# Kernel tuning notes

Measured on AMD Instinct MI355X. Metric: run time of the kernel, lower is better.

## Reference

```python
import jax, jax.numpy as jnp
import numpy as np

N_HEADS = 16
NEG_INF = -1e9


def setup_inputs() -> dict:
    key = jax.random.key(0)
    k1, k2, k3 = jax.random.split(key, 3)
    B, S, D = 4, 4096, 1024
    x = jax.random.normal(k1, (B, S, D), dtype=jnp.float32)
    # GPT-2-style init scale
    w_qkv = jax.random.normal(k2, (D, 3 * D), dtype=jnp.float32) * 0.02
    b_qkv = jnp.zeros((3 * D,), dtype=jnp.float32)
    w_o = jax.random.normal(k3, (D, D), dtype=jnp.float32) * 0.02
    b_o = jnp.zeros((D,), dtype=jnp.float32)
    return {"x": x, "w_qkv": w_qkv, "b_qkv": b_qkv, "w_o": w_o, "b_o": b_o,
            "window_size": 512}


def reference(x, w_qkv, b_qkv, w_o, b_o, window_size):
    B, S, D = x.shape
    W = window_size
    n_win = S // W  # loop `for i in range(0, S, W)` with S % W == 0
    H = N_HEADS
    dh = D // H

    # All windows are independent -> fold them into the batch dim instead of a
    # Python loop (same math as looping + concat along seq dim).
    xw = x.reshape(B * n_win, W, D)

    qkv = xw @ w_qkv + b_qkv                      # [BN, W, 3D]
    q, k, v = jnp.split(qkv, 3, axis=-1)
    # [BN, H, W, dh]
    q = q.reshape(-1, W, H, dh).transpose(0, 2, 1, 3)
    k = k.reshape(-1, W, H, dh).transpose(0, 2, 1, 3)
    v = v.reshape(-1, W, H, dh).transpose(0, 2, 1, 3)

    scale = 1.0 / jnp.sqrt(jnp.asarray(dh, dtype=x.dtype))
    scores = jnp.einsum('bhqd,bhkd->bhqk', q, k) * scale  # [BN, H, W, W]
    causal = jnp.tril(jnp.ones((W, W), dtype=bool))       # GPT-2 causal mask (per window)
    scores = jnp.where(causal, scores, NEG_INF)
    attn = jax.nn.softmax(scores, axis=-1)

    out = jnp.einsum('bhqk,bhkd->bhqd', attn, v)          # [BN, H, W, dh]
    out = out.transpose(0, 2, 1, 3).reshape(-1, W, D)     # [BN, W, D]
    out = out @ w_o + b_o
    return out.reshape(B, S, D)
```

## Files before the change

kernel.cpp:

```cpp
#include <hip/hip_runtime.h>


typedef unsigned short u16;
typedef unsigned int u32;
typedef __attribute__((ext_vector_type(8))) short bf16x8;
typedef __attribute__((ext_vector_type(4))) float f32x4;

__device__ __forceinline__ float bf2f(u16 v) {
  union { u32 u; float f; } t; t.u = ((u32)v) << 16; return t.f;
}
__device__ __forceinline__ u16 f2bf(float f) {
  union { float f; u32 u; } t; t.f = f;
  u32 u = t.u + 0x7fffu + ((t.u >> 16) & 1u);
  return (u16)(u >> 16);
}
__device__ __forceinline__ void g2lds16(const void* g, void* l) {
  __builtin_amdgcn_global_load_lds((const __attribute__((address_space(1))) void*)g,
                                   (__attribute__((address_space(3))) void*)l,
                                   16, 0, 0);
}

__global__ __launch_bounds__(256) void canon_x(
    const float* __restrict__ xf, u16* __restrict__ xb) {
  size_t i = ((size_t)blockIdx.x * 256 + threadIdx.x) * 8;
  float4 a = *(const float4*)(xf + i);
  float4 b = *(const float4*)(xf + i + 4);
  u16 o[8] = { f2bf(a.x), f2bf(a.y), f2bf(a.z), f2bf(a.w),
               f2bf(b.x), f2bf(b.y), f2bf(b.z), f2bf(b.w) };
  *(bf16x8*)(xb + i) = *(bf16x8*)o;
}

__global__ __launch_bounds__(256) void transpose_w(
    const float* __restrict__ in, u16* __restrict__ out, int R, int C) {
  __shared__ u16 tile[32][33];
  int c0 = blockIdx.x * 32, r0 = blockIdx.y * 32;
  int tx = threadIdx.x & 31, ty = threadIdx.x >> 5;
#pragma unroll
  for (int i = 0; i < 32; i += 8)
    tile[ty + i][tx] = f2bf(in[(size_t)(r0 + ty + i) * C + c0 + tx]);
  __syncthreads();
#pragma unroll
  for (int i = 0; i < 32; i += 8)
    out[(size_t)(c0 + ty + i) * R + r0 + tx] = tile[tx][ty + i];
}

__global__ __launch_bounds__(256) void transpose_v(
    const u16* __restrict__ qkv, u16* __restrict__ vt) {
  __shared__ u16 tile[32][33];
  int bh = blockIdx.z, bn = bh >> 4, h = bh & 15;
  int t0 = blockIdx.x * 32, d0 = blockIdx.y * 32;
  int tx = threadIdx.x & 31, ty = threadIdx.x >> 5;
  const u16* src = qkv + (size_t)(bn * 512) * 3072 + 2048 + h * 64;
#pragma unroll
  for (int i = 0; i < 32; i += 8)
    tile[ty + i][tx] = src[(size_t)(t0 + ty + i) * 3072 + d0 + tx];
  __syncthreads();
  u16* dst = vt + ((size_t)bh * 64 + d0) * 512 + t0;
#pragma unroll
  for (int i = 0; i < 32; i += 8)
    dst[(size_t)(ty + i) * 512 + tx] = tile[tx][ty + i];
}

template <typename OutT>
__global__ __launch_bounds__(256, 2) void gemm_bt_bias(
    const u16* __restrict__ A, const u16* __restrict__ Bt,
    const float* __restrict__ bias, OutT* __restrict__ C,
    int M, int N, int K) {
  __shared__ __align__(16) u16 As[128 * 32];
  __shared__ __align__(16) u16 Bs[128 * 32];
  const int tid = threadIdx.x;
  const int wave = tid >> 6, lane = tid & 63;
  const int quad = lane >> 4, l16 = lane & 15;
  const int m0 = blockIdx.y * 128, n0 = blockIdx.x * 128;
  const int wm = (wave >> 1) * 64, wn = (wave & 1) * 64;

  f32x4 acc[4][4] = {};

  int e0 = (wave * 512) + lane * 8;
  int e1 = 2048 + e0;
  int rA0 = e0 >> 5, cA0 = e0 & 31;
  int rA1 = e1 >> 5, cA1 = e1 & 31;
  const u16* ga0 = A + (size_t)(m0 + rA0) * K + cA0;
  const u16* ga1 = A + (size_t)(m0 + rA1) * K + cA1;
  const u16* gb0 = Bt + (size_t)(n0 + rA0) * K + cA0;
  const u16* gb1 = Bt + (size_t)(n0 + rA1) * K + cA1;
  u16* As0 = As + (size_t)wave * 512;
  u16* As1 = As0 + 2048;
  u16* Bs0 = Bs + (size_t)wave * 512;
  u16* Bs1 = Bs0 + 2048;

  for (int k0 = 0; k0 < K; k0 += 32) {
    g2lds16(ga0 + k0, As0);
    g2lds16(ga1 + k0, As1);
    g2lds16(gb0 + k0, Bs0);
    g2lds16(gb1 + k0, Bs1);
    __syncthreads();
    bf16x8 a[4], b[4];
#pragma unroll
    for (int mi = 0; mi < 4; ++mi)
      a[mi] = *(const bf16x8*)(As + (wm + mi * 16 + l16) * 32 + quad * 8);
#pragma unroll
    for (int ni = 0; ni < 4; ++ni)
      b[ni] = *(const bf16x8*)(Bs + (wn + ni * 16 + l16) * 32 + quad * 8);
#pragma unroll
    for (int mi = 0; mi < 4; ++mi)
#pragma unroll
      for (int ni = 0; ni < 4; ++ni)
        acc[mi][ni] = __builtin_amdgcn_mfma_f32_16x16x32_bf16(a[mi], b[ni], acc[mi][ni], 0, 0, 0);
    __syncthreads();
  }

#pragma unroll
  for (int ni = 0; ni < 4; ++ni) {
    int col = n0 + wn + ni * 16 + l16;
    float bv = bias[col];
#pragma unroll
    for (int mi = 0; mi < 4; ++mi) {
      int row = m0 + wm + mi * 16 + quad * 4;
#pragma unroll
      for (int r = 0; r < 4; ++r) {
        float v = acc[mi][ni][r] + bv;
        if constexpr (sizeof(OutT) == 2)
          C[(size_t)(row + r) * N + col] = f2bf(v);
        else
          C[(size_t)(row + r) * N + col] = v;
      }
    }
  }
}

__global__ __launch_bounds__(256, 2) void attn_win(
    const u16* __restrict__ qkv, const u16* __restrict__ vt,
    u16* __restrict__ attn) {
  __shared__ __align__(16) u16 Qs[128 * 64];
  __shared__ __align__(16) u16 Ks[128 * 64];
  __shared__ __align__(16) u16 Vs[64 * 128];
  __shared__ __align__(16) u16 Ps[4][32 * 128];

  const int qt = blockIdx.x, h = blockIdx.y, bn = blockIdx.z;
  const int bh = bn * 16 + h;
  const int tid = threadIdx.x;
  const int wave = tid >> 6, lane = tid & 63;
  const int quad = lane >> 4, l16 = lane & 15;
  const int t0 = bn * 512 + qt * 128;

#pragma unroll
  for (int it = 0; it < 4; ++it) {
    int i = it * 256 + tid;
    int row = i >> 3, c = i & 7;
    bf16x8 v = *(const bf16x8*)(qkv + (size_t)(t0 + row) * 3072 + h * 64 + c * 8);
    *(bf16x8*)(Qs + row * 64 + ((c ^ (row & 7)) * 8)) = v;
  }

  float mrun[2][4], lrun[2][4];
  f32x4 o[2][4] = {};
#pragma unroll
  for (int mi = 0; mi < 2; ++mi)
#pragma unroll
    for (int r = 0; r < 4; ++r) { mrun[mi][r] = -1e30f; lrun[mi][r] = 0.f; }

  const float cexp = 0.18033688011112042f;

  for (int j = 0; j <= qt; ++j) {
    int tk = bn * 512 + j * 128;
#pragma unroll
    for (int it = 0; it < 4; ++it) {
      int i = it * 256 + tid;
      int rk = i >> 3, ck = i & 7;
      bf16x8 kv = *(const bf16x8*)(qkv + (size_t)(tk + rk) * 3072 + 1024 + h * 64 + ck * 8);
      *(bf16x8*)(Ks + rk * 64 + ((ck ^ (rk & 7)) * 8)) = kv;
      int rv = i >> 4, cv = i & 15;
      bf16x8 vv = *(const bf16x8*)(vt + ((size_t)bh * 64 + rv) * 512 + j * 128 + cv * 8);
      *(bf16x8*)(Vs + rv * 128 + ((cv ^ (rv & 15)) * 8)) = vv;
    }
    __syncthreads();

    f32x4 s[2][8] = {};
#pragma unroll
    for (int ks = 0; ks < 2; ++ks) {
      bf16x8 aq[2];
#pragma unroll
      for (int mi = 0; mi < 2; ++mi) {
        int m = wave * 32 + mi * 16 + l16;
        aq[mi] = *(const bf16x8*)(Qs + m * 64 + (((ks * 4 + quad) ^ (m & 7)) * 8));
      }
#pragma unroll
      for (int ni = 0; ni < 8; ++ni) {
        int n = ni * 16 + l16;
        bf16x8 bk = *(const bf16x8*)(Ks + n * 64 + (((ks * 4 + quad) ^ (n & 7)) * 8));
        s[0][ni] = __builtin_amdgcn_mfma_f32_16x16x32_bf16(aq[0], bk, s[0][ni], 0, 0, 0);
        s[1][ni] = __builtin_amdgcn_mfma_f32_16x16x32_bf16(aq[1], bk, s[1][ni], 0, 0, 0);
      }
    }

    const bool diag = (j == qt);
#pragma unroll
    for (int mi = 0; mi < 2; ++mi) {
#pragma unroll
      for (int r = 0; r < 4; ++r) {
        int m = wave * 32 + mi * 16 + quad * 4 + r;
        float rmax = -1e30f;
#pragma unroll
        for (int ni = 0; ni < 8; ++ni) {
          float v = s[mi][ni][r] * cexp;
          if (diag && (ni * 16 + l16 > m)) v = -1e30f;
          s[mi][ni][r] = v;
          rmax = fmaxf(rmax, v);
        }
        rmax = fmaxf(rmax, __shfl_xor(rmax, 1));
        rmax = fmaxf(rmax, __shfl_xor(rmax, 2));
        rmax = fmaxf(rmax, __shfl_xor(rmax, 4));
        rmax = fmaxf(rmax, __shfl_xor(rmax, 8));
        float mnew = fmaxf(mrun[mi][r], rmax);
        float alpha = exp2f(mrun[mi][r] - mnew);
        mrun[mi][r] = mnew;
        float rsum = 0.f;
#pragma unroll
        for (int ni = 0; ni < 8; ++ni) {
          float pv = exp2f(s[mi][ni][r] - mnew);
          s[mi][ni][r] = pv;
          rsum += pv;
        }
        rsum += __shfl_xor(rsum, 1);
        rsum += __shfl_xor(rsum, 2);
        rsum += __shfl_xor(rsum, 4);
        rsum += __shfl_xor(rsum, 8);
        lrun[mi][r] = lrun[mi][r] * alpha + rsum;
#pragma unroll
        for (int di = 0; di < 4; ++di) o[mi][di][r] *= alpha;
      }
    }

    u16* pw = &Ps[wave][0];
#pragma unroll
    for (int mi = 0; mi < 2; ++mi)
#pragma unroll
      for (int ni = 0; ni < 8; ++ni)
#pragma unroll
        for (int r = 0; r < 4; ++r) {
          int row = mi * 16 + quad * 4 + r;
          int col = ni * 16 + l16;
          int phys = (col >> 3) ^ (row & 15);
          pw[row * 128 + phys * 8 + (col & 7)] = f2bf(s[mi][ni][r]);
        }
    __syncthreads();

#pragma unroll
    for (int ks = 0; ks < 4; ++ks) {
      bf16x8 ap[2];
#pragma unroll
      for (int mi = 0; mi < 2; ++mi) {
        int row = mi * 16 + l16;
        ap[mi] = *(const bf16x8*)(pw + row * 128 + (((ks * 4 + quad) ^ (row & 15)) * 8));
      }
#pragma unroll
      for (int di = 0; di < 4; ++di) {
        int n = di * 16 + l16;
        bf16x8 bv = *(const bf16x8*)(Vs + n * 128 + (((ks * 4 + quad) ^ (n & 15)) * 8));
        o[0][di] = __builtin_amdgcn_mfma_f32_16x16x32_bf16(ap[0], bv, o[0][di], 0, 0, 0);
        o[1][di] = __builtin_amdgcn_mfma_f32_16x16x32_bf16(ap[1], bv, o[1][di], 0, 0, 0);
      }
    }
    __syncthreads();
  }

#pragma unroll
  for (int mi = 0; mi < 2; ++mi)
#pragma unroll
    for (int r = 0; r < 4; ++r) {
      float inv = 1.0f / lrun[mi][r];
      int trow = t0 + wave * 32 + mi * 16 + quad * 4 + r;
#pragma unroll
      for (int di = 0; di < 4; ++di)
        attn[(size_t)trow * 1024 + h * 64 + di * 16 + l16] = f2bf(o[mi][di][r] * inv);
    }
}

extern "C" void kernel_launch(void* const* d_in, const int* in_sizes, int n_in,
                              void* d_out, int out_size, void* d_ws, size_t ws_size,
                              hipStream_t stream) {
  (void)in_sizes; (void)n_in; (void)out_size; (void)ws_size;
  const float* x     = (const float*)d_in[0];
  const float* w_qkv = (const float*)d_in[1];
  const float* b_qkv = (const float*)d_in[2];
  const float* w_o   = (const float*)d_in[3];
  const float* b_o   = (const float*)d_in[4];
  float* out = (float*)d_out;

  char* ws = (char*)d_ws;
  u16* qkv   = (u16*)(ws + 0);
  u16* vtb   = (u16*)(ws + 100663296);
  u16* attnb = (u16*)(ws + 134217728);
  u16* xb    = (u16*)(ws + 167772160);
  u16* wqkvT = (u16*)(ws + 201326592);
  u16* woT   = (u16*)(ws + 207618048);

  canon_x<<<8192, 256, 0, stream>>>(x, xb);
  transpose_w<<<dim3(96, 32), 256, 0, stream>>>(w_qkv, wqkvT, 1024, 3072);
  transpose_w<<<dim3(32, 32), 256, 0, stream>>>(w_o, woT, 1024, 1024);

  gemm_bt_bias<u16><<<dim3(24, 128), 256, 0, stream>>>(
      xb, wqkvT, b_qkv, qkv, 16384, 3072, 1024);
  transpose_v<<<dim3(16, 2, 512), 256, 0, stream>>>(qkv, vtb);
  attn_win<<<dim3(4, 16, 32), 256, 0, stream>>>(qkv, vtb, attnb);
  gemm_bt_bias<float><<<dim3(8, 128), 256, 0, stream>>>(
      attnb, woT, b_o, out, 16384, 1024, 1024);
}
```

Baseline: 464.8 us.

## Read Q/K/V fragments directly from global memory and fold softmax scale into QKV GEMM

The attention kernel no longer stages Q, K and V tiles through shared memory. Q fragments are kept in registers and K/V fragments are loaded straight from global memory into MFMA operands, which removes the block-wide barriers and cuts LDS use so three blocks per CU can run. The softmax scale (with log2e) is applied in the QKV GEMM epilogue to the Q columns, dropping a multiply per score. In exchange, each wave now reads K/V from global or L2 on its own instead of sharing one staged copy, and the bf16 rounding of Q now happens after scaling.

```diff
diff --git a/kernel.cpp b/kernel.cpp
--- a/kernel.cpp
+++ b/kernel.cpp
@@ -65,7 +65,7 @@
 __global__ __launch_bounds__(256, 2) void gemm_bt_bias(
     const u16* __restrict__ A, const u16* __restrict__ Bt,
     const float* __restrict__ bias, OutT* __restrict__ C,
-    int M, int N, int K) {
+    int M, int N, int K, int qcols, float qscale) {
   __shared__ __align__(16) u16 As[128 * 32];
   __shared__ __align__(16) u16 Bs[128 * 32];
   const int tid = threadIdx.x;
@@ -114,12 +114,13 @@
   for (int ni = 0; ni < 4; ++ni) {
     int col = n0 + wn + ni * 16 + l16;
     float bv = bias[col];
+    float sc = (col < qcols) ? qscale : 1.0f;
 #pragma unroll
     for (int mi = 0; mi < 4; ++mi) {
       int row = m0 + wm + mi * 16 + quad * 4;
 #pragma unroll
       for (int r = 0; r < 4; ++r) {
-        float v = acc[mi][ni][r] + bv;
+        float v = (acc[mi][ni][r] + bv) * sc;
         if constexpr (sizeof(OutT) == 2)
           C[(size_t)(row + r) * N + col] = f2bf(v);
         else
@@ -129,28 +130,25 @@
   }
 }
 
-__global__ __launch_bounds__(256, 2) void attn_win(
+__global__ __launch_bounds__(256, 3) void attn_win(
     const u16* __restrict__ qkv, const u16* __restrict__ vt,
     u16* __restrict__ attn) {
-  __shared__ __align__(16) u16 Qs[128 * 64];
-  __shared__ __align__(16) u16 Ks[128 * 64];
-  __shared__ __align__(16) u16 Vs[64 * 128];
   __shared__ __align__(16) u16 Ps[4][32 * 128];
 
   const int qt = blockIdx.x, h = blockIdx.y, bn = blockIdx.z;
   const int bh = bn * 16 + h;
-  const int tid = threadIdx.x;
-  const int wave = tid >> 6, lane = tid & 63;
+  const int wave = threadIdx.x >> 6, lane = threadIdx.x & 63;
   const int quad = lane >> 4, l16 = lane & 15;
   const int t0 = bn * 512 + qt * 128;
-
-#pragma unroll
-  for (int it = 0; it < 4; ++it) {
-    int i = it * 256 + tid;
-    int row = i >> 3, c = i & 7;
-    bf16x8 v = *(const bf16x8*)(qkv + (size_t)(t0 + row) * 3072 + h * 64 + c * 8);
-    *(bf16x8*)(Qs + row * 64 + ((c ^ (row & 7)) * 8)) = v;
-  }
+  const int qrow = t0 + wave * 32;
+
+  bf16x8 qf[2][2];
+#pragma unroll
+  for (int mi = 0; mi < 2; ++mi)
+#pragma unroll
+    for (int ks = 0; ks < 2; ++ks)
+      qf[mi][ks] = *(const bf16x8*)(
+          qkv + (size_t)(qrow + mi * 16 + l16) * 3072 + h * 64 + ks * 32 + quad * 8);
 
   float mrun[2][4], lrun[2][4];
   f32x4 o[2][4] = {};
@@ -159,39 +157,21 @@
 #pragma unroll
     for (int r = 0; r < 4; ++r) { mrun[mi][r] = -1e30f; lrun[mi][r] = 0.f; }
 
-  const float cexp = 0.18033688011112042f;
+  u16* pw = &Ps[wave][0];
 
   for (int j = 0; j <= qt; ++j) {
-    int tk = bn * 512 + j * 128;
-#pragma unroll
-    for (int it = 0; it < 4; ++it) {
-      int i = it * 256 + tid;
-      int rk = i >> 3, ck = i & 7;
-      bf16x8 kv = *(const bf16x8*)(qkv + (size_t)(tk + rk) * 3072 + 1024 + h * 64 + ck * 8);
-      *(bf16x8*)(Ks + rk * 64 + ((ck ^ (rk & 7)) * 8)) = kv;
-      int rv = i >> 4, cv = i & 15;
-      bf16x8 vv = *(const bf16x8*)(vt + ((size_t)bh * 64 + rv) * 512 + j * 128 + cv * 8);
-      *(bf16x8*)(Vs + rv * 128 + ((cv ^ (rv & 15)) * 8)) = vv;
-    }
-    __syncthreads();
+    const u16* kbase = qkv + (size_t)(bn * 512 + j * 128) * 3072 + 1024 + h * 64;
 
     f32x4 s[2][8] = {};
 #pragma unroll
-    for (int ks = 0; ks < 2; ++ks) {
-      bf16x8 aq[2];
-#pragma unroll
-      for (int mi = 0; mi < 2; ++mi) {
-        int m = wave * 32 + mi * 16 + l16;
-        aq[mi] = *(const bf16x8*)(Qs + m * 64 + (((ks * 4 + quad) ^ (m & 7)) * 8));
-      }
+    for (int ks = 0; ks < 2; ++ks)
 #pragma unroll
       for (int ni = 0; ni < 8; ++ni) {
-        int n = ni * 16 + l16;
-        bf16x8 bk = *(const bf16x8*)(Ks + n * 64 + (((ks * 4 + quad) ^ (n & 7)) * 8));
-        s[0][ni] = __builtin_amdgcn_mfma_f32_16x16x32_bf16(aq[0], bk, s[0][ni], 0, 0, 0);
-        s[1][ni] = __builtin_amdgcn_mfma_f32_16x16x32_bf16(aq[1], bk, s[1][ni], 0, 0, 0);
-      }
-    }
+        bf16x8 bk = *(const bf16x8*)(
+            kbase + (size_t)(ni * 16 + l16) * 3072 + ks * 32 + quad * 8);
+        s[0][ni] = __builtin_amdgcn_mfma_f32_16x16x32_bf16(qf[0][ks], bk, s[0][ni], 0, 0, 0);
+        s[1][ni] = __builtin_amdgcn_mfma_f32_16x16x32_bf16(qf[1][ks], bk, s[1][ni], 0, 0, 0);
+      }
 
     const bool diag = (j == qt);
 #pragma unroll
@@ -202,7 +182,7 @@
         float rmax = -1e30f;
 #pragma unroll
         for (int ni = 0; ni < 8; ++ni) {
-          float v = s[mi][ni][r] * cexp;
+          float v = s[mi][ni][r];
           if (diag && (ni * 16 + l16 > m)) v = -1e30f;
           s[mi][ni][r] = v;
           rmax = fmaxf(rmax, v);
@@ -231,7 +211,6 @@
       }
     }
 
-    u16* pw = &Ps[wave][0];
 #pragma unroll
     for (int mi = 0; mi < 2; ++mi)
 #pragma unroll
@@ -243,8 +222,8 @@
           int phys = (col >> 3) ^ (row & 15);
           pw[row * 128 + phys * 8 + (col & 7)] = f2bf(s[mi][ni][r]);
         }
-    __syncthreads();
-
+
+    const u16* vbase = vt + (size_t)bh * 64 * 512 + j * 128;
 #pragma unroll
     for (int ks = 0; ks < 4; ++ks) {
       bf16x8 ap[2];
@@ -255,13 +234,12 @@
       }
 #pragma unroll
       for (int di = 0; di < 4; ++di) {
-        int n = di * 16 + l16;
-        bf16x8 bv = *(const bf16x8*)(Vs + n * 128 + (((ks * 4 + quad) ^ (n & 15)) * 8));
+        bf16x8 bv = *(const bf16x8*)(
+            vbase + (size_t)(di * 16 + l16) * 512 + ks * 32 + quad * 8);
         o[0][di] = __builtin_amdgcn_mfma_f32_16x16x32_bf16(ap[0], bv, o[0][di], 0, 0, 0);
         o[1][di] = __builtin_amdgcn_mfma_f32_16x16x32_bf16(ap[1], bv, o[1][di], 0, 0, 0);
       }
     }
-    __syncthreads();
   }
 
 #pragma unroll
@@ -295,14 +273,16 @@
   u16* wqkvT = (u16*)(ws + 201326592);
   u16* woT   = (u16*)(ws + 207618048);
 
+  const float cexp = 0.18033688011112042f;
+
   canon_x<<<8192, 256, 0, stream>>>(x, xb);
   transpose_w<<<dim3(96, 32), 256, 0, stream>>>(w_qkv, wqkvT, 1024, 3072);
   transpose_w<<<dim3(32, 32), 256, 0, stream>>>(w_o, woT, 1024, 1024);
 
   gemm_bt_bias<u16><<<dim3(24, 128), 256, 0, stream>>>(
-      xb, wqkvT, b_qkv, qkv, 16384, 3072, 1024);
+      xb, wqkvT, b_qkv, qkv, 16384, 3072, 1024, 1024, cexp);
   transpose_v<<<dim3(16, 2, 512), 256, 0, stream>>>(qkv, vtb);
   attn_win<<<dim3(4, 16, 32), 256, 0, stream>>>(qkv, vtb, attnb);
   gemm_bt_bias<float><<<dim3(8, 128), 256, 0, stream>>>(
-      attnb, woT, b_o, out, 16384, 1024, 1024);
-}
+      attnb, woT, b_o, out, 16384, 1024, 1024, 0, 1.0f);
+}
```

New measurement: 712.9 us. +53.4%, slower.
